# Optimization experiments

Hardware: AMD Instinct MI355X
Metric: run time of the kernel (lower is better)

## Reference

```python
import jax, jax.numpy as jnp
import numpy as np

D = 1024        # d_model
H = 4           # num_heads
DK = D          # key_dim   (expand_k = 1.0)
DV = 2 * D      # value_dim (expand_v = 2.0)
HK = DK // H    # per-head key dim
HV = DV // H    # per-head value dim
KCONV = 4       # short conv kernel size
EPS = 1e-5
CHUNK = 64      # scan chunk size (checkpointing granularity)


def causal_conv_silu(x, w):
    # x: [B,T,C], w: [C,K] depthwise causal conv followed by silu
    B, T, C = x.shape
    K = w.shape[1]
    xp = jnp.pad(x, ((0, 0), (K - 1, 0), (0, 0)))
    y = sum(xp[:, i:i + T, :] * w[:, i] for i in range(K))
    return jax.nn.silu(y)


def l2norm(x):
    return x * jax.lax.rsqrt(jnp.sum(x * x, -1, keepdims=True) + 1e-6)


def _step(S, inp):
    # gated delta rule, one time step. S: [B,H,HK,HV]
    q_t, k_t, v_t, g_t, b_t = inp  # [B,H,HK],[B,H,HK],[B,H,HV],[B,H],[B,H]
    S = S * jnp.exp(g_t)[..., None, None]
    v_eff = (v_t - jnp.einsum('bhk,bhkv->bhv', k_t, S)) * b_t[..., None]
    S = S + k_t[..., None] * v_eff[..., None, :]
    o_t = jnp.einsum('bhk,bhkv->bhv', q_t, S)
    return S, o_t


@jax.checkpoint
def _chunk(S, ch):
    return jax.lax.scan(_step, S, ch)


def _forward(x, ln_w, ln_b, Wq, Wk, Wv, conv_q, conv_k, conv_v, Wb, Wa,
             A_log, dt_bias, Wg, norm_w, Wo):
    B, T, _ = x.shape
    # pre-LayerNorm
    mu = jnp.mean(x, -1, keepdims=True)
    var = jnp.mean((x - mu) ** 2, -1, keepdims=True)
    normed = (x - mu) * jax.lax.rsqrt(var + EPS) * ln_w + ln_b
    # projections + short conv + silu
    q = causal_conv_silu(normed @ Wq, conv_q)
    k = causal_conv_silu(normed @ Wk, conv_k)
    v = causal_conv_silu(normed @ Wv, conv_v)
    beta = jax.nn.sigmoid(normed @ Wb)                                # [B,T,H]
    g = -jnp.exp(A_log) * jax.nn.softplus(normed @ Wa + dt_bias)      # [B,T,H]
    q = l2norm(q.reshape(B, T, H, HK)) * (HK ** -0.5)
    k = l2norm(k.reshape(B, T, H, HK))
    v = v.reshape(B, T, H, HV)
    # chunked sequential scan over time
    nc = T // CHUNK
    def to_chunks(a):
        return jnp.moveaxis(a, 1, 0).reshape((nc, CHUNK, B) + a.shape[2:])
    qc, kc, vc, gc, bc = map(to_chunks, (q, k, v, g, beta))
    S0 = jnp.zeros((B, H, HK, HV), x.dtype)
    _, o = jax.lax.scan(_chunk, S0, (qc, kc, vc, gc, bc))
    o = jnp.moveaxis(o.reshape(T, B, H, HV), 0, 1)                    # [B,T,H,HV]
    # RMSNorm-swish output gate
    g_out = (normed @ Wg).reshape(B, T, H, HV)
    o = o * jax.lax.rsqrt(jnp.mean(o * o, -1, keepdims=True) + EPS) * norm_w
    o = o * g_out * jax.nn.sigmoid(g_out)
    return x + o.reshape(B, T, DV) @ Wo


def setup_inputs() -> dict:
    key = jax.random.key(0)
    ks = jax.random.split(key, 16)
    B, T = 4, 2048
    p = lambda k, shape, s=0.02: jax.random.normal(k, shape, jnp.float32) * s
    return {
        'x': jax.random.normal(ks[0], (B, T, D), jnp.float32),
        'ln_w': jnp.ones((D,), jnp.float32),
        'ln_b': jnp.zeros((D,), jnp.float32),
        'Wq': p(ks[1], (D, DK)),
        'Wk': p(ks[2], (D, DK)),
        'Wv': p(ks[3], (D, DV)),
        'conv_q': p(ks[4], (DK, KCONV), 0.1),
        'conv_k': p(ks[5], (DK, KCONV), 0.1),
        'conv_v': p(ks[6], (DV, KCONV), 0.1),
        'Wb': p(ks[7], (D, H)),
        'Wa': p(ks[8], (D, H)),
        'A_log': jnp.log(jax.random.uniform(ks[9], (H,), jnp.float32, 1.0, 16.0)),
        'dt_bias': jnp.log(jnp.expm1(jax.random.uniform(ks[10], (H,), jnp.float32, 0.001, 0.1))),
        'Wg': p(ks[11], (D, DV)),
        'norm_w': jnp.ones((HV,), jnp.float32),
        'Wo': p(ks[12], (DV, D)),
    }


def reference(x, ln_w, ln_b, Wq, Wk, Wv, conv_q, conv_k, conv_v, Wb, Wa,
              A_log, dt_bias, Wg, norm_w, Wo):
    return _forward(x, ln_w, ln_b, Wq, Wk, Wv, conv_q, conv_k, conv_v,
                    Wb, Wa, A_log, dt_bias, Wg, norm_w, Wo)
```

## Files before the change

### kernel.cpp

```cpp
#include <hip/hip_runtime.h>
#include <math.h>

#define BB 4
#define TT 2048
#define RTOT 8192
#define DD 1024
#define HH 4
#define DKC 1024
#define DVC 2048
#define HKC 256
#define HVC 512
#define NC 32
#define TILE_CV 32

typedef unsigned short u16;
typedef unsigned int u32;
typedef short bf8v __attribute__((ext_vector_type(8)));
typedef float f32x4 __attribute__((ext_vector_type(4)));

__device__ __forceinline__ float bf2f(u16 u) {
    union { float f; u32 i; } c; c.i = ((u32)u) << 16; return c.f;
}
__device__ __forceinline__ u16 f2bf(float f) {
    union { float f; u32 i; } c; c.f = f;
    const u32 i = c.i;
    return (u16)((i + 0x7FFFu + ((i >> 16) & 1u)) >> 16);
}
__device__ __forceinline__ float sigmoidf_(float x) { return 1.0f / (1.0f + expf(-x)); }
__device__ __forceinline__ f32x4 mfma16(bf8v a, bf8v b, f32x4 c) {
    return __builtin_amdgcn_mfma_f32_16x16x32_bf16(a, b, c, 0, 0, 0);
}

__global__ __launch_bounds__(256) void ln_kernel(const float* __restrict__ x,
                                                 const float* __restrict__ w,
                                                 const float* __restrict__ b,
                                                 u16* __restrict__ out) {
    const int row = blockIdx.x;
    const int tid = threadIdx.x;
    const int lane = tid & 63, wave = tid >> 6;
    const float4 xv = *(const float4*)&x[(size_t)row * DD + tid * 4];
    float s = xv.x + xv.y + xv.z + xv.w;
    float sq = xv.x * xv.x + xv.y * xv.y + xv.z * xv.z + xv.w * xv.w;
    for (int m = 32; m >= 1; m >>= 1) {
        s += __shfl_xor(s, m, 64);
        sq += __shfl_xor(sq, m, 64);
    }
    __shared__ float s1[4], s2[4];
    if (lane == 0) { s1[wave] = s; s2[wave] = sq; }
    __syncthreads();
    const float tot = s1[0] + s1[1] + s1[2] + s1[3];
    const float totq = s2[0] + s2[1] + s2[2] + s2[3];
    const float mean = tot * (1.0f / DD);
    const float var = totq * (1.0f / DD) - mean * mean;
    const float rstd = rsqrtf(var + 1e-5f);
    const float4 wv = *(const float4*)&w[tid * 4];
    const float4 bv = *(const float4*)&b[tid * 4];
    ushort4 o;
    o.x = f2bf((xv.x - mean) * rstd * wv.x + bv.x);
    o.y = f2bf((xv.y - mean) * rstd * wv.y + bv.y);
    o.z = f2bf((xv.z - mean) * rstd * wv.z + bv.z);
    o.w = f2bf((xv.w - mean) * rstd * wv.w + bv.w);
    *(ushort4*)&out[(size_t)row * DD + tid * 4] = o;
}

__global__ __launch_bounds__(256) void wconv_kernel(const float* __restrict__ W,
                                                    u16* __restrict__ WT, int K, int N) {
    __shared__ float tile[32][33];
    const int k0 = blockIdx.x * 32, n0 = blockIdx.y * 32;
    const int t = threadIdx.x;
    const int r = t >> 3, c4 = (t & 7) * 4;
    const float4 v = *(const float4*)&W[(size_t)(k0 + r) * N + n0 + c4];
    tile[r][c4 + 0] = v.x; tile[r][c4 + 1] = v.y;
    tile[r][c4 + 2] = v.z; tile[r][c4 + 3] = v.w;
    __syncthreads();
    ushort4 o;
    o.x = f2bf(tile[c4 + 0][r]); o.y = f2bf(tile[c4 + 1][r]);
    o.z = f2bf(tile[c4 + 2][r]); o.w = f2bf(tile[c4 + 3][r]);
    *(ushort4*)&WT[(size_t)(n0 + r) * K + k0 + c4] = o;
}

template <int OUTMODE>
__global__ __launch_bounds__(256, 2) void gemm_mfma(const u16* __restrict__ A,
                                                    const u16* __restrict__ BT,
                                                    void* __restrict__ Cv,
                                                    int M, int N, int K,
                                                    const float* __restrict__ Res) {
    __shared__ u16 As[128][40];
    __shared__ u16 Bs[128][40];
    const int tid = threadIdx.x;
    const int wave = tid >> 6, lane = tid & 63;
    const int quad = lane >> 4, l15 = lane & 15;
    const int wr = wave >> 1, wc = wave & 1;
    const int bn = blockIdx.x, bm = blockIdx.y;
    const int srow = tid >> 1, sh = (tid & 1) * 16;
    const u16* Ap = A + (size_t)(bm * 128 + srow) * K + sh;
    const u16* Bp = BT + (size_t)(bn * 128 + srow) * K + sh;
    f32x4 acc[4][4];
#pragma unroll
    for (int i = 0; i < 4; ++i)
#pragma unroll
        for (int j = 0; j < 4; ++j) acc[i][j] = (f32x4){0.f, 0.f, 0.f, 0.f};

    for (int k0 = 0; k0 < K; k0 += 32) {
        const bf8v a0 = *(const bf8v*)(Ap + k0);
        const bf8v a1 = *(const bf8v*)(Ap + k0 + 8);
        const bf8v b0 = *(const bf8v*)(Bp + k0);
        const bf8v b1 = *(const bf8v*)(Bp + k0 + 8);
        __syncthreads();
        *(bf8v*)&As[srow][sh] = a0;
        *(bf8v*)&As[srow][sh + 8] = a1;
        *(bf8v*)&Bs[srow][sh] = b0;
        *(bf8v*)&Bs[srow][sh + 8] = b1;
        __syncthreads();
        bf8v af[4], bfr[4];
#pragma unroll
        for (int i = 0; i < 4; ++i) af[i] = *(const bf8v*)&As[wr * 64 + i * 16 + l15][quad * 8];
#pragma unroll
        for (int j = 0; j < 4; ++j) bfr[j] = *(const bf8v*)&Bs[wc * 64 + j * 16 + l15][quad * 8];
#pragma unroll
        for (int i = 0; i < 4; ++i)
#pragma unroll
            for (int j = 0; j < 4; ++j)
                acc[i][j] = mfma16(af[i], bfr[j], acc[i][j]);
    }
#pragma unroll
    for (int i = 0; i < 4; ++i) {
        const int row = bm * 128 + wr * 64 + i * 16 + quad * 4;
#pragma unroll
        for (int j = 0; j < 4; ++j) {
            const int col = bn * 128 + wc * 64 + j * 16 + l15;
            if (OUTMODE == 0) {
                u16* C = (u16*)Cv;
#pragma unroll
                for (int r = 0; r < 4; ++r)
                    C[(size_t)(row + r) * N + col] = f2bf(acc[i][j][r]);
            } else {
                float* C = (float*)Cv;
#pragma unroll
                for (int r = 0; r < 4; ++r)
                    C[(size_t)(row + r) * N + col] = acc[i][j][r] + Res[(size_t)(row + r) * N + col];
            }
        }
    }
}

__global__ __launch_bounds__(256) void smallproj_kernel(const float* __restrict__ x,
                                                        const float* __restrict__ lnw,
                                                        const float* __restrict__ lnb,
                                                        const float* __restrict__ Wb,
                                                        const float* __restrict__ Wa,
                                                        const float* __restrict__ A_log,
                                                        const float* __restrict__ dt_bias,
                                                        float* __restrict__ beta,
                                                        float* __restrict__ gdec) {
    const int row = blockIdx.x;
    const int tid = threadIdx.x;
    const int lane = tid & 63, wave = tid >> 6;
    const float4 xv = *(const float4*)&x[(size_t)row * DD + tid * 4];
    float s = xv.x + xv.y + xv.z + xv.w;
    float sq = xv.x * xv.x + xv.y * xv.y + xv.z * xv.z + xv.w * xv.w;
    for (int m = 32; m >= 1; m >>= 1) {
        s += __shfl_xor(s, m, 64);
        sq += __shfl_xor(sq, m, 64);
    }
    __shared__ float s1[4], s2[4];
    if (lane == 0) { s1[wave] = s; s2[wave] = sq; }
    __syncthreads();
    const float mean = (s1[0] + s1[1] + s1[2] + s1[3]) * (1.0f / DD);
    const float var = (s2[0] + s2[1] + s2[2] + s2[3]) * (1.0f / DD) - mean * mean;
    const float rstd = rsqrtf(var + 1e-5f);
    const float4 wv = *(const float4*)&lnw[tid * 4];
    const float4 bv = *(const float4*)&lnb[tid * 4];
    float nv[4];
    nv[0] = (xv.x - mean) * rstd * wv.x + bv.x;
    nv[1] = (xv.y - mean) * rstd * wv.y + bv.y;
    nv[2] = (xv.z - mean) * rstd * wv.z + bv.z;
    nv[3] = (xv.w - mean) * rstd * wv.w + bv.w;
    float acc[8] = {};
#pragma unroll
    for (int j = 0; j < 4; ++j) {
        const int kk = tid * 4 + j;
        const float4 wb = ((const float4*)Wb)[kk];
        const float4 wa = ((const float4*)Wa)[kk];
        acc[0] += nv[j] * wb.x; acc[1] += nv[j] * wb.y; acc[2] += nv[j] * wb.z; acc[3] += nv[j] * wb.w;
        acc[4] += nv[j] * wa.x; acc[5] += nv[j] * wa.y; acc[6] += nv[j] * wa.z; acc[7] += nv[j] * wa.w;
    }
#pragma unroll
    for (int i = 0; i < 8; ++i)
        for (int m = 32; m >= 1; m >>= 1) acc[i] += __shfl_xor(acc[i], m, 64);
    __shared__ float sred[4][8];
    if (lane == 0)
#pragma unroll
        for (int i = 0; i < 8; ++i) sred[wave][i] = acc[i];
    __syncthreads();
    if (tid < 8) {
        const float sv = sred[0][tid] + sred[1][tid] + sred[2][tid] + sred[3][tid];
        if (tid < 4) {
            beta[(size_t)row * HH + tid] = 1.0f / (1.0f + expf(-sv));
        } else {
            const int h = tid - 4;
            const float z = sv + dt_bias[h];
            const float sp = (z > 20.0f) ? z : log1pf(expf(z));
            gdec[(size_t)row * HH + h] = -expf(A_log[h]) * sp;
        }
    }
}

__global__ __launch_bounds__(256) void halo_save(const u16* __restrict__ P,
                                                 u16* __restrict__ halo, int C) {
    const int tt = blockIdx.x;
    const int r0 = tt * TILE_CV;
    const int t0 = r0 & (TT - 1);
    const int n4 = (3 * C) >> 2;
    for (int idx = threadIdx.x; idx < n4; idx += 256) {
        const int flat = idx * 4;
        const int j = flat / C;
        const int c = flat - j * C;
        ushort4 vv;
        if (t0 == 0) { vv.x = vv.y = vv.z = vv.w = 0; }
        else vv = *(const ushort4*)&P[(size_t)(r0 - 1 - j) * C + c];
        *(ushort4*)&halo[(size_t)(tt * 3 + j) * C + c] = vv;
    }
}

__global__ __launch_bounds__(256) void conv_inplace(u16* __restrict__ P,
                                                    const float* __restrict__ w,
                                                    const u16* __restrict__ halo, int C) {
    const int tt = blockIdx.y;
    const int r0 = tt * TILE_CV;
    const int c0 = blockIdx.x * 1024 + threadIdx.x * 4;
    float wt[4][4];
#pragma unroll
    for (int j = 0; j < 4; ++j)
#pragma unroll
        for (int i = 0; i < 4; ++i) wt[j][i] = w[(c0 + j) * 4 + i];
    float xm1[4], xm2[4], xm3[4];
    {
        const ushort4 h0 = *(const ushort4*)&halo[(size_t)(tt * 3 + 0) * C + c0];
        const ushort4 h1 = *(const ushort4*)&halo[(size_t)(tt * 3 + 1) * C + c0];
        const ushort4 h2 = *(const ushort4*)&halo[(size_t)(tt * 3 + 2) * C + c0];
        xm1[0] = bf2f(h0.x); xm1[1] = bf2f(h0.y); xm1[2] = bf2f(h0.z); xm1[3] = bf2f(h0.w);
        xm2[0] = bf2f(h1.x); xm2[1] = bf2f(h1.y); xm2[2] = bf2f(h1.z); xm2[3] = bf2f(h1.w);
        xm3[0] = bf2f(h2.x); xm3[1] = bf2f(h2.y); xm3[2] = bf2f(h2.z); xm3[3] = bf2f(h2.w);
    }
    for (int t = 0; t < TILE_CV; ++t) {
        u16* rowp = P + (size_t)(r0 + t) * C + c0;
        const ushort4 cv = *(const ushort4*)rowp;
        float cur[4] = {bf2f(cv.x), bf2f(cv.y), bf2f(cv.z), bf2f(cv.w)};
        ushort4 ov;
        u16* op = (u16*)&ov;
#pragma unroll
        for (int j = 0; j < 4; ++j) {
            const float y = xm3[j] * wt[j][0] + xm2[j] * wt[j][1] + xm1[j] * wt[j][2] + cur[j] * wt[j][3];
            op[j] = f2bf(y * sigmoidf_(y));
        }
        *(ushort4*)rowp = ov;
#pragma unroll
        for (int j = 0; j < 4; ++j) { xm3[j] = xm2[j]; xm2[j] = xm1[j]; xm1[j] = cur[j]; }
    }
}

__global__ __launch_bounds__(256) void normqk_kernel(u16* __restrict__ q, u16* __restrict__ k) {
    const int row = blockIdx.x;
    const int tid = threadIdx.x;
    const int h = tid >> 6, lane = tid & 63;
    const size_t base = (size_t)row * DKC + h * HKC + lane * 4;
    const ushort4 q4 = *(ushort4*)&q[base];
    const ushort4 k4 = *(ushort4*)&k[base];
    float qv[4] = {bf2f(q4.x), bf2f(q4.y), bf2f(q4.z), bf2f(q4.w)};
    float kv[4] = {bf2f(k4.x), bf2f(k4.y), bf2f(k4.z), bf2f(k4.w)};
    float sq = qv[0]*qv[0] + qv[1]*qv[1] + qv[2]*qv[2] + qv[3]*qv[3];
    float sk = kv[0]*kv[0] + kv[1]*kv[1] + kv[2]*kv[2] + kv[3]*kv[3];
    for (int m = 32; m >= 1; m >>= 1) {
        sq += __shfl_xor(sq, m, 64);
        sk += __shfl_xor(sk, m, 64);
    }
    const float qs = rsqrtf(sq + 1e-6f) * 0.0625f;
    const float ks = rsqrtf(sk + 1e-6f);
    ushort4 qo, ko;
    qo.x = f2bf(qv[0]*qs); qo.y = f2bf(qv[1]*qs); qo.z = f2bf(qv[2]*qs); qo.w = f2bf(qv[3]*qs);
    ko.x = f2bf(kv[0]*ks); ko.y = f2bf(kv[1]*ks); ko.z = f2bf(kv[2]*ks); ko.w = f2bf(kv[3]*ks);
    *(ushort4*)&q[base] = qo;
    *(ushort4*)&k[base] = ko;
}

__global__ __launch_bounds__(256) void p1a_kernel(const u16* __restrict__ qg,
                                                  const u16* __restrict__ kg,
                                                  const float* __restrict__ gdec,
                                                  const float* __restrict__ beta,
                                                  u16* __restrict__ Mg,
                                                  u16* __restrict__ Pg,
                                                  float* __restrict__ gcg) {
    __shared__ float T[64][68];
    __shared__ float Mm[64][68];
    __shared__ float gcs[64], bars[64];
    const int CI = blockIdx.x;
    const int c = CI & 31, h = (CI >> 5) & 3, b = CI >> 7;
    const int tid = threadIdx.x, lane = tid & 63, wave = tid >> 6;
    const int quad = lane >> 4, l15 = lane & 15;
    const int rowbase = b * TT + c * 64;
    if (wave == 0) {
        float g = gdec[(size_t)(rowbase + lane) * HH + h];
        for (int d = 1; d < 64; d <<= 1) { float o2 = __shfl_up(g, d, 64); if (lane >= d) g += o2; }
        gcs[lane] = g;
        bars[lane] = beta[(size_t)(rowbase + lane) * HH + h];
        gcg[CI * 64 + lane] = g;
    }
    __syncthreads();
    const int t0 = wave * 16;
    f32x4 kk[4], qk[4];
#pragma unroll
    for (int st = 0; st < 4; ++st) { kk[st] = (f32x4){0,0,0,0}; qk[st] = (f32x4){0,0,0,0}; }
    const size_t arow = (size_t)(rowbase + t0 + l15) * DKC + h * HKC + quad * 8;
    for (int ks = 0; ks < 8; ++ks) {
        const bf8v ak = *(const bf8v*)(kg + arow + ks * 32);
        const bf8v aq = *(const bf8v*)(qg + arow + ks * 32);
#pragma unroll
        for (int st = 0; st < 4; ++st) {
            const size_t brow = (size_t)(rowbase + st * 16 + l15) * DKC + h * HKC + quad * 8 + ks * 32;
            const bf8v bk = *(const bf8v*)(kg + brow);
            kk[st] = mfma16(ak, bk, kk[st]);
            qk[st] = mfma16(aq, bk, qk[st]);
        }
    }
#pragma unroll
    for (int st = 0; st < 4; ++st)
#pragma unroll
        for (int i = 0; i < 4; ++i) {
            const int t = t0 + quad * 4 + i, s = st * 16 + l15;
            const float e = expf(gcs[t] - gcs[s]);
            T[t][s] = (s < t) ? bars[t] * e * kk[st][i] : 0.f;
            Pg[(size_t)CI * 4096 + t * 64 + s] = f2bf((s <= t) ? e * qk[st][i] : 0.f);
        }
    __syncthreads();
    if (wave == 0) {
        const int j = lane;
        Mm[0][j] = (j == 0) ? 1.f : 0.f;
        for (int t = 1; t < 64; ++t) {
            float acc = 0.f;
            for (int s = 0; s < t; ++s) acc += T[t][s] * Mm[s][j];
            Mm[t][j] = ((t == j) ? 1.f : 0.f) - acc;
        }
    }
    __syncthreads();
    for (int idx = tid; idx < 4096; idx += 256)
        Mg[(size_t)CI * 4096 + idx] = f2bf(Mm[idx >> 6][idx & 63]);
}

__global__ __launch_bounds__(256) void p2_kernel(const u16* __restrict__ qg,
                                                 const u16* __restrict__ kg,
                                                 const u16* __restrict__ vg,
                                                 const float* __restrict__ beta,
                                                 const float* __restrict__ gcg,
                                                 const u16* __restrict__ Mg,
                                                 const u16* __restrict__ Pg,
                                                 u16* __restrict__ og) {
    __shared__ u16 SbT[32][264];
    __shared__ u16 buf[18432];
    __shared__ u16 tT[32][72];
    __shared__ float barr[64], negbg[64], gamt[64], gcdg[64];
    __shared__ float gCsh;
    const int bid = blockIdx.x;
    const int vs = bid & 15, h = (bid >> 4) & 3, b = bid >> 6;
    const int tid = threadIdx.x, lane = tid & 63, wave = tid >> 6;
    const int quad = lane >> 4, l15 = lane & 15;
    const int t0 = wave * 16;
    for (int i = tid; i < 32 * 264; i += 256) ((u16*)SbT)[i] = 0;
    f32x4 S[4][2];
#pragma unroll
    for (int a = 0; a < 4; ++a)
#pragma unroll
        for (int nb = 0; nb < 2; ++nb) S[a][nb] = (f32x4){0,0,0,0};

    const int srow = tid >> 2, scq = tid & 3;

    for (int c = 0; c < NC; ++c) {
        const int CI = (b * 4 + h) * NC + c;
        const int rowbase = b * TT + c * 64;
        __syncthreads();
        if (wave == 0) {
            const float gc = gcg[CI * 64 + lane];
            const float gc63 = __shfl(gc, 63, 64);
            const float bt = beta[(size_t)(rowbase + lane) * HH + h];
            const float gt = expf(gc);
            barr[lane] = bt; gamt[lane] = gt;
            negbg[lane] = -bt * gt;
            gcdg[lane] = expf(gc63 - gc);
            if (lane == 0) gCsh = expf(gc63);
        }
        __syncthreads();
        {
            const float sc = negbg[srow];
            const u16* krow = kg + (size_t)(rowbase + srow) * DKC + h * HKC + scq * 64;
            u16* dst = buf + srow * 264 + scq * 64;
#pragma unroll
            for (int it = 0; it < 8; ++it) {
                const ushort4 a0 = *(const ushort4*)(krow + it * 8);
                const ushort4 a1 = *(const ushort4*)(krow + it * 8 + 4);
                ushort4 o0, o1;
                o0.x = f2bf(bf2f(a0.x)*sc); o0.y = f2bf(bf2f(a0.y)*sc);
                o0.z = f2bf(bf2f(a0.z)*sc); o0.w = f2bf(bf2f(a0.w)*sc);
                o1.x = f2bf(bf2f(a1.x)*sc); o1.y = f2bf(bf2f(a1.y)*sc);
                o1.z = f2bf(bf2f(a1.z)*sc); o1.w = f2bf(bf2f(a1.w)*sc);
                *(ushort4*)(dst + it * 8) = o0;
                *(ushort4*)(dst + it * 8 + 4) = o1;
            }
        }
        __syncthreads();
        f32x4 uacc[2];
#pragma unroll
        for (int nb = 0; nb < 2; ++nb) {
            f32x4 ci;
#pragma unroll
            for (int i = 0; i < 4; ++i) {
                const int t = t0 + quad * 4 + i;
                ci[i] = barr[t] * bf2f(vg[(size_t)(rowbase + t) * DVC + h * HVC + vs * 32 + nb * 16 + l15]);
            }
            uacc[nb] = ci;
        }
        for (int ks = 0; ks < 8; ++ks) {
            const bf8v af = *(const bf8v*)(buf + (t0 + l15) * 264 + ks * 32 + quad * 8);
#pragma unroll
            for (int nb = 0; nb < 2; ++nb) {
                const bf8v bf_ = *(const bf8v*)(&SbT[nb * 16 + l15][ks * 32 + quad * 8]);
                uacc[nb] = mfma16(af, bf_, uacc[nb]);
            }
        }
#pragma unroll
        for (int nb = 0; nb < 2; ++nb) {
            ushort4 p;
            p.x = f2bf(uacc[nb][0]); p.y = f2bf(uacc[nb][1]);
            p.z = f2bf(uacc[nb][2]); p.w = f2bf(uacc[nb][3]);
            *(ushort4*)(&tT[nb * 16 + l15][t0 + quad * 4]) = p;
        }
        __syncthreads();
        f32x4 vacc[2] = {(f32x4){0,0,0,0}, (f32x4){0,0,0,0}};
        for (int ks = 0; ks < 2; ++ks) {
            const bf8v am = *(const bf8v*)(Mg + (size_t)CI * 4096 + (t0 + l15) * 64 + ks * 32 + quad * 8);
#pragma unroll
            for (int nb = 0; nb < 2; ++nb) {
                const bf8v bu = *(const bf8v*)(&tT[nb * 16 + l15][ks * 32 + quad * 8]);
                vacc[nb] = mfma16(am, bu, vacc[nb]);
            }
        }
        {
            const float sc = gamt[srow];
            const u16* qrow = qg + (size_t)(rowbase + srow) * DKC + h * HKC + scq * 64;
            u16* dst = buf + srow * 264 + scq * 64;
#pragma unroll
            for (int it = 0; it < 8; ++it) {
                const ushort4 a0 = *(const ushort4*)(qrow + it * 8);
                const ushort4 a1 = *(const ushort4*)(qrow + it * 8 + 4);
                ushort4 o0, o1;
                o0.x = f2bf(bf2f(a0.x)*sc); o0.y = f2bf(bf2f(a0.y)*sc);
                o0.z = f2bf(bf2f(a0.z)*sc); o0.w = f2bf(bf2f(a0.w)*sc);
                o1.x = f2bf(bf2f(a1.x)*sc); o1.y = f2bf(bf2f(a1.y)*sc);
                o1.z = f2bf(bf2f(a1.z)*sc); o1.w = f2bf(bf2f(a1.w)*sc);
                *(ushort4*)(dst + it * 8) = o0;
                *(ushort4*)(dst + it * 8 + 4) = o1;
            }
        }
        __syncthreads();
#pragma unroll
        for (int nb = 0; nb < 2; ++nb) {
            ushort4 p;
            p.x = f2bf(vacc[nb][0]); p.y = f2bf(vacc[nb][1]);
            p.z = f2bf(vacc[nb][2]); p.w = f2bf(vacc[nb][3]);
            *(ushort4*)(&tT[nb * 16 + l15][t0 + quad * 4]) = p;
        }
        __syncthreads();
        f32x4 oacc[2] = {(f32x4){0,0,0,0}, (f32x4){0,0,0,0}};
        for (int ks = 0; ks < 2; ++ks) {
            const bf8v ap = *(const bf8v*)(Pg + (size_t)CI * 4096 + (t0 + l15) * 64 + ks * 32 + quad * 8);
#pragma unroll
            for (int nb = 0; nb < 2; ++nb) {
                const bf8v bv_ = *(const bf8v*)(&tT[nb * 16 + l15][ks * 32 + quad * 8]);
                oacc[nb] = mfma16(ap, bv_, oacc[nb]);
            }
        }
        for (int ks = 0; ks < 8; ++ks) {
            const bf8v af = *(const bf8v*)(buf + (t0 + l15) * 264 + ks * 32 + quad * 8);
#pragma unroll
            for (int nb = 0; nb < 2; ++nb) {
                const bf8v bs = *(const bf8v*)(&SbT[nb * 16 + l15][ks * 32 + quad * 8]);
                oacc[nb] = mfma16(af, bs, oacc[nb]);
            }
        }
#pragma unroll
        for (int nb = 0; nb < 2; ++nb)
#pragma unroll
            for (int i = 0; i < 4; ++i) {
                const int t = t0 + quad * 4 + i;
                og[((size_t)(b * 4 + h) * TT + c * 64 + t) * HVC + vs * 32 + nb * 16 + l15] = f2bf(oacc[nb][i]);
            }
        __syncthreads();
        {
            const float sc = gcdg[srow];
            const u16* krow = kg + (size_t)(rowbase + srow) * DKC + h * HKC + scq * 64;
#pragma unroll
            for (int it = 0; it < 8; ++it) {
                const ushort4 a0 = *(const ushort4*)(krow + it * 8);
                const ushort4 a1 = *(const ushort4*)(krow + it * 8 + 4);
                const int cbase = scq * 64 + it * 8;
                buf[(cbase + 0) * 72 + srow] = f2bf(bf2f(a0.x)*sc);
                buf[(cbase + 1) * 72 + srow] = f2bf(bf2f(a0.y)*sc);
                buf[(cbase + 2) * 72 + srow] = f2bf(bf2f(a0.z)*sc);
                buf[(cbase + 3) * 72 + srow] = f2bf(bf2f(a0.w)*sc);
                buf[(cbase + 4) * 72 + srow] = f2bf(bf2f(a1.x)*sc);
                buf[(cbase + 5) * 72 + srow] = f2bf(bf2f(a1.y)*sc);
                buf[(cbase + 6) * 72 + srow] = f2bf(bf2f(a1.z)*sc);
                buf[(cbase + 7) * 72 + srow] = f2bf(bf2f(a1.w)*sc);
            }
        }
        __syncthreads();
        const float gC = gCsh;
#pragma unroll
        for (int a = 0; a < 4; ++a) {
            const int r0 = (wave * 4 + a) * 16;
#pragma unroll
            for (int nb = 0; nb < 2; ++nb) {
                f32x4 acc = S[a][nb] * gC;
                for (int ks = 0; ks < 2; ++ks) {
                    const bf8v akt = *(const bf8v*)(buf + (r0 + l15) * 72 + ks * 32 + quad * 8);
                    const bf8v bv_ = *(const bf8v*)(&tT[nb * 16 + l15][ks * 32 + quad * 8]);
                    acc = mfma16(akt, bv_, acc);
                }
                S[a][nb] = acc;
                ushort4 p;
                p.x = f2bf(acc[0]); p.y = f2bf(acc[1]);
                p.z = f2bf(acc[2]); p.w = f2bf(acc[3]);
                *(ushort4*)(&SbT[nb * 16 + l15][r0 + quad * 4]) = p;
            }
        }
    }
}

__global__ __launch_bounds__(256) void gate_kernel(const u16* __restrict__ o,
                                                   u16* __restrict__ pg,
                                                   const float* __restrict__ norm_w) {
    const int row = blockIdx.x;
    const int b = row >> 11, t = row & 2047;
    const int tid = threadIdx.x;
    const int h = tid >> 6, lane = tid & 63;
    const size_t obase = ((size_t)(b * 4 + h) * TT + t) * HVC + lane * 4;
    const size_t pbase = (size_t)row * DVC + h * HVC + lane * 4;
    const ushort4 a4 = *(const ushort4*)&o[obase];
    const ushort4 b4 = *(const ushort4*)&o[obase + 256];
    float o1[4] = {bf2f(a4.x), bf2f(a4.y), bf2f(a4.z), bf2f(a4.w)};
    float o2[4] = {bf2f(b4.x), bf2f(b4.y), bf2f(b4.z), bf2f(b4.w)};
    float ss = 0.f;
#pragma unroll
    for (int j = 0; j < 4; ++j) ss += o1[j]*o1[j] + o2[j]*o2[j];
    for (int m = 32; m >= 1; m >>= 1) ss += __shfl_xor(ss, m, 64);
    const float rms = rsqrtf(ss * (1.0f / HVC) + 1e-5f);
    const float4 nw1 = *(const float4*)&norm_w[lane * 4];
    const float4 nw2 = *(const float4*)&norm_w[256 + lane * 4];
    const ushort4 g4a = *(const ushort4*)&pg[pbase];
    const ushort4 g4b = *(const ushort4*)&pg[pbase + 256];
    const float g1[4] = {bf2f(g4a.x), bf2f(g4a.y), bf2f(g4a.z), bf2f(g4a.w)};
    const float g2[4] = {bf2f(g4b.x), bf2f(g4b.y), bf2f(g4b.z), bf2f(g4b.w)};
    const float n1[4] = {nw1.x, nw1.y, nw1.z, nw1.w};
    const float n2[4] = {nw2.x, nw2.y, nw2.z, nw2.w};
    ushort4 r1, r2;
    u16* p1 = (u16*)&r1; u16* p2 = (u16*)&r2;
#pragma unroll
    for (int j = 0; j < 4; ++j) {
        p1[j] = f2bf(o1[j] * rms * n1[j] * g1[j] * sigmoidf_(g1[j]));
        p2[j] = f2bf(o2[j] * rms * n2[j] * g2[j] * sigmoidf_(g2[j]));
    }
    *(ushort4*)&pg[pbase] = r1;
    *(ushort4*)&pg[pbase + 256] = r2;
}

extern "C" void kernel_launch(void* const* d_in, const int* in_sizes, int n_in,
                              void* d_out, int out_size, void* d_ws, size_t ws_size,
                              hipStream_t stream) {
    const float* x       = (const float*)d_in[0];
    const float* ln_w    = (const float*)d_in[1];
    const float* ln_b    = (const float*)d_in[2];
    const float* Wq      = (const float*)d_in[3];
    const float* Wk      = (const float*)d_in[4];
    const float* Wv      = (const float*)d_in[5];
    const float* conv_q  = (const float*)d_in[6];
    const float* conv_k  = (const float*)d_in[7];
    const float* conv_v  = (const float*)d_in[8];
    const float* Wb      = (const float*)d_in[9];
    const float* Wa      = (const float*)d_in[10];
    const float* A_log   = (const float*)d_in[11];
    const float* dt_bias = (const float*)d_in[12];
    const float* Wg      = (const float*)d_in[13];
    const float* norm_w  = (const float*)d_in[14];
    const float* Wo      = (const float*)d_in[15];
    float* out = (float*)d_out;

    char* ws = (char*)d_ws;
    u16* normed = (u16*)(ws);
    u16* q      = (u16*)(ws + (16ull << 20));
    u16* k      = (u16*)(ws + (32ull << 20));
    u16* v      = (u16*)(ws + (48ull << 20));
    u16* o      = (u16*)(ws + (80ull << 20));
    float* beta = (float*)(ws + (112ull << 20));
    float* gdec = (float*)(ws + (112ull << 20) + (128u<<10));
    float* gcg  = (float*)(ws + (112ull << 20) + (256u<<10));
    u16* halo   = (u16*)(ws + (113ull << 20));
    u16* Mg     = (u16*)(ws + (116ull << 20));
    u16* Pg     = (u16*)(ws + (120ull << 20));
    u16* pg     = q;
    u16* WTe    = o;
    u16* WgT    = Mg;
    u16* WoT    = v;

    ln_kernel<<<RTOT, 256, 0, stream>>>(x, ln_w, ln_b, normed);

    wconv_kernel<<<dim3(DD / 32, DKC / 32), 256, 0, stream>>>(Wq, WTe, DD, DKC);
    gemm_mfma<0><<<dim3(DKC / 128, RTOT / 128), 256, 0, stream>>>(normed, WTe, q, RTOT, DKC, DD, nullptr);
    wconv_kernel<<<dim3(DD / 32, DKC / 32), 256, 0, stream>>>(Wk, WTe, DD, DKC);
    gemm_mfma<0><<<dim3(DKC / 128, RTOT / 128), 256, 0, stream>>>(normed, WTe, k, RTOT, DKC, DD, nullptr);
    wconv_kernel<<<dim3(DD / 32, DVC / 32), 256, 0, stream>>>(Wv, WTe, DD, DVC);
    gemm_mfma<0><<<dim3(DVC / 128, RTOT / 128), 256, 0, stream>>>(normed, WTe, v, RTOT, DVC, DD, nullptr);
    smallproj_kernel<<<RTOT, 256, 0, stream>>>(x, ln_w, ln_b, Wb, Wa, A_log, dt_bias, beta, gdec);

    halo_save<<<RTOT / TILE_CV, 256, 0, stream>>>(q, halo, DKC);
    conv_inplace<<<dim3(1, RTOT / TILE_CV), 256, 0, stream>>>(q, conv_q, halo, DKC);
    halo_save<<<RTOT / TILE_CV, 256, 0, stream>>>(k, halo, DKC);
    conv_inplace<<<dim3(1, RTOT / TILE_CV), 256, 0, stream>>>(k, conv_k, halo, DKC);
    halo_save<<<RTOT / TILE_CV, 256, 0, stream>>>(v, halo, DVC);
    conv_inplace<<<dim3(2, RTOT / TILE_CV), 256, 0, stream>>>(v, conv_v, halo, DVC);

    normqk_kernel<<<RTOT, 256, 0, stream>>>(q, k);

    p1a_kernel<<<BB * HH * NC, 256, 0, stream>>>(q, k, gdec, beta, Mg, Pg, gcg);
    p2_kernel<<<BB * HH * (HVC / 32), 256, 0, stream>>>(q, k, v, beta, gcg, Mg, Pg, o);

    wconv_kernel<<<dim3(DD / 32, DVC / 32), 256, 0, stream>>>(Wg, WgT, DD, DVC);
    gemm_mfma<0><<<dim3(DVC / 128, RTOT / 128), 256, 0, stream>>>(normed, WgT, pg, RTOT, DVC, DD, nullptr);

    gate_kernel<<<RTOT, 256, 0, stream>>>(o, pg, norm_w);

    wconv_kernel<<<dim3(DVC / 32, DD / 32), 256, 0, stream>>>(Wo, WoT, DVC, DD);
    gemm_mfma<1><<<dim3(DD / 128, RTOT / 128), 256, 0, stream>>>(pg, WoT, out, RTOT, DD, DVC, x);
}
```

Before: 792.5 us.

## Restructure chunk recurrence kernel with double-buffered state and precomputed transposed keys

```diff
diff --git a/kernel.cpp b/kernel.cpp
--- a/kernel.cpp
+++ b/kernel.cpp
@@ -290,6 +290,7 @@
                                                   const float* __restrict__ beta,
                                                   u16* __restrict__ Mg,
                                                   u16* __restrict__ Pg,
+                                                  u16* __restrict__ kTg,
                                                   float* __restrict__ gcg) {
     __shared__ float T[64][68];
     __shared__ float Mm[64][68];
@@ -308,6 +309,12 @@
     }
     __syncthreads();
     const int t0 = wave * 16;
+    bf8v I0, I16;
+#pragma unroll
+    for (int j = 0; j < 8; ++j) {
+        ((u16*)&I0)[j]  = (quad * 8 + j == l15)      ? (u16)0x3F80 : (u16)0;
+        ((u16*)&I16)[j] = (quad * 8 + j == l15 + 16) ? (u16)0x3F80 : (u16)0;
+    }
     f32x4 kk[4], qk[4];
 #pragma unroll
     for (int st = 0; st < 4; ++st) { kk[st] = (f32x4){0,0,0,0}; qk[st] = (f32x4){0,0,0,0}; }
@@ -315,6 +322,15 @@
     for (int ks = 0; ks < 8; ++ks) {
         const bf8v ak = *(const bf8v*)(kg + arow + ks * 32);
         const bf8v aq = *(const bf8v*)(qg + arow + ks * 32);
+        f32x4 tr0 = (f32x4){0,0,0,0}, tr1 = (f32x4){0,0,0,0};
+        tr0 = mfma16(I0, ak, tr0);
+        tr1 = mfma16(I16, ak, tr1);
+        const size_t kbase = (size_t)CI * 16384 + t0 + l15;
+#pragma unroll
+        for (int i = 0; i < 4; ++i) {
+            kTg[kbase + (size_t)(ks * 32 + quad * 4 + i) * 64] = f2bf(tr0[i]);
+            kTg[kbase + (size_t)(ks * 32 + 16 + quad * 4 + i) * 64] = f2bf(tr1[i]);
+        }
 #pragma unroll
         for (int st = 0; st < 4; ++st) {
             const size_t brow = (size_t)(rowbase + st * 16 + l15) * DKC + h * HKC + quad * 8 + ks * 32;
@@ -347,191 +363,123 @@
         Mg[(size_t)CI * 4096 + idx] = f2bf(Mm[idx >> 6][idx & 63]);
 }
 
-__global__ __launch_bounds__(256) void p2_kernel(const u16* __restrict__ qg,
+__global__ __launch_bounds__(512) void p2_kernel(const u16* __restrict__ qg,
                                                  const u16* __restrict__ kg,
                                                  const u16* __restrict__ vg,
                                                  const float* __restrict__ beta,
                                                  const float* __restrict__ gcg,
                                                  const u16* __restrict__ Mg,
                                                  const u16* __restrict__ Pg,
+                                                 const u16* __restrict__ kTg,
                                                  u16* __restrict__ og) {
-    __shared__ u16 SbT[32][264];
-    __shared__ u16 buf[18432];
-    __shared__ u16 tT[32][72];
-    __shared__ float barr[64], negbg[64], gamt[64], gcdg[64];
-    __shared__ float gCsh;
+    __shared__ u16 SbT[2][32][264];
+    __shared__ u16 uT[32][72];
+    __shared__ u16 vT[32][72];
+    __shared__ u16 v2T[32][72];
     const int bid = blockIdx.x;
     const int vs = bid & 15, h = (bid >> 4) & 3, b = bid >> 6;
     const int tid = threadIdx.x, lane = tid & 63, wave = tid >> 6;
     const int quad = lane >> 4, l15 = lane & 15;
-    const int t0 = wave * 16;
-    for (int i = tid; i < 32 * 264; i += 256) ((u16*)SbT)[i] = 0;
-    f32x4 S[4][2];
-#pragma unroll
-    for (int a = 0; a < 4; ++a)
-#pragma unroll
-        for (int nb = 0; nb < 2; ++nb) S[a][nb] = (f32x4){0,0,0,0};
-
-    const int srow = tid >> 2, scq = tid & 3;
+    const int tw = wave >> 1, nw = wave & 1;
+    const int t0 = tw * 16;
+    const int ncol = nw * 16 + l15;
+    for (int i = tid; i < 32 * 264; i += 512) ((u16*)SbT[0])[i] = 0;
+    f32x4 S[4];
+#pragma unroll
+    for (int a = 0; a < 4; ++a) S[a] = (f32x4){0,0,0,0};
+    __syncthreads();
 
     for (int c = 0; c < NC; ++c) {
+        const int cur = c & 1, nxt = cur ^ 1;
         const int CI = (b * 4 + h) * NC + c;
         const int rowbase = b * TT + c * 64;
-        __syncthreads();
-        if (wave == 0) {
-            const float gc = gcg[CI * 64 + lane];
-            const float gc63 = __shfl(gc, 63, 64);
-            const float bt = beta[(size_t)(rowbase + lane) * HH + h];
-            const float gt = expf(gc);
-            barr[lane] = bt; gamt[lane] = gt;
-            negbg[lane] = -bt * gt;
-            gcdg[lane] = expf(gc63 - gc);
-            if (lane == 0) gCsh = expf(gc63);
-        }
-        __syncthreads();
+        const float gc63 = gcg[CI * 64 + 63];
+        float bt[4], ga[4], gd[4];
+#pragma unroll
+        for (int i = 0; i < 4; ++i) {
+            const int t = t0 + quad * 4 + i;
+            bt[i] = beta[(size_t)(rowbase + t) * HH + h];
+            const float gc = gcg[CI * 64 + t];
+            ga[i] = expf(gc);
+            gd[i] = expf(gc63 - gc);
+        }
+        const size_t krow = (size_t)(rowbase + t0 + l15) * DKC + h * HKC + quad * 8;
+        f32x4 ka0 = (f32x4){0,0,0,0}, ka1 = (f32x4){0,0,0,0};
+        for (int ks = 0; ks < 8; ks += 2) {
+            const bf8v ak0 = *(const bf8v*)(kg + krow + ks * 32);
+            const bf8v ak1 = *(const bf8v*)(kg + krow + ks * 32 + 32);
+            const bf8v bs0 = *(const bf8v*)(&SbT[cur][ncol][ks * 32 + quad * 8]);
+            const bf8v bs1 = *(const bf8v*)(&SbT[cur][ncol][ks * 32 + 32 + quad * 8]);
+            ka0 = mfma16(ak0, bs0, ka0);
+            ka1 = mfma16(ak1, bs1, ka1);
+        }
         {
-            const float sc = negbg[srow];
-            const u16* krow = kg + (size_t)(rowbase + srow) * DKC + h * HKC + scq * 64;
-            u16* dst = buf + srow * 264 + scq * 64;
-#pragma unroll
-            for (int it = 0; it < 8; ++it) {
-                const ushort4 a0 = *(const ushort4*)(krow + it * 8);
-                const ushort4 a1 = *(const ushort4*)(krow + it * 8 + 4);
-                ushort4 o0, o1;
-                o0.x = f2bf(bf2f(a0.x)*sc); o0.y = f2bf(bf2f(a0.y)*sc);
-                o0.z = f2bf(bf2f(a0.z)*sc); o0.w = f2bf(bf2f(a0.w)*sc);
-                o1.x = f2bf(bf2f(a1.x)*sc); o1.y = f2bf(bf2f(a1.y)*sc);
-                o1.z = f2bf(bf2f(a1.z)*sc); o1.w = f2bf(bf2f(a1.w)*sc);
-                *(ushort4*)(dst + it * 8) = o0;
-                *(ushort4*)(dst + it * 8 + 4) = o1;
-            }
-        }
-        __syncthreads();
-        f32x4 uacc[2];
-#pragma unroll
-        for (int nb = 0; nb < 2; ++nb) {
-            f32x4 ci;
+            ushort4 up; u16* upp = (u16*)&up;
 #pragma unroll
             for (int i = 0; i < 4; ++i) {
                 const int t = t0 + quad * 4 + i;
-                ci[i] = barr[t] * bf2f(vg[(size_t)(rowbase + t) * DVC + h * HVC + vs * 32 + nb * 16 + l15]);
+                const float vv = bf2f(vg[(size_t)(rowbase + t) * DVC + h * HVC + vs * 32 + ncol]);
+                upp[i] = f2bf(bt[i] * vv - bt[i] * ga[i] * (ka0[i] + ka1[i]));
             }
-            uacc[nb] = ci;
-        }
-        for (int ks = 0; ks < 8; ++ks) {
-            const bf8v af = *(const bf8v*)(buf + (t0 + l15) * 264 + ks * 32 + quad * 8);
-#pragma unroll
-            for (int nb = 0; nb < 2; ++nb) {
-                const bf8v bf_ = *(const bf8v*)(&SbT[nb * 16 + l15][ks * 32 + quad * 8]);
-                uacc[nb] = mfma16(af, bf_, uacc[nb]);
-            }
-        }
-#pragma unroll
-        for (int nb = 0; nb < 2; ++nb) {
-            ushort4 p;
-            p.x = f2bf(uacc[nb][0]); p.y = f2bf(uacc[nb][1]);
-            p.z = f2bf(uacc[nb][2]); p.w = f2bf(uacc[nb][3]);
-            *(ushort4*)(&tT[nb * 16 + l15][t0 + quad * 4]) = p;
+            *(ushort4*)(&uT[ncol][t0 + quad * 4]) = up;
         }
         __syncthreads();
-        f32x4 vacc[2] = {(f32x4){0,0,0,0}, (f32x4){0,0,0,0}};
+        f32x4 vacc = (f32x4){0,0,0,0};
         for (int ks = 0; ks < 2; ++ks) {
             const bf8v am = *(const bf8v*)(Mg + (size_t)CI * 4096 + (t0 + l15) * 64 + ks * 32 + quad * 8);
-#pragma unroll
-            for (int nb = 0; nb < 2; ++nb) {
-                const bf8v bu = *(const bf8v*)(&tT[nb * 16 + l15][ks * 32 + quad * 8]);
-                vacc[nb] = mfma16(am, bu, vacc[nb]);
+            const bf8v bu = *(const bf8v*)(&uT[ncol][ks * 32 + quad * 8]);
+            vacc = mfma16(am, bu, vacc);
+        }
+        {
+            ushort4 vp, v2p; u16* vpp = (u16*)&vp; u16* v2pp = (u16*)&v2p;
+#pragma unroll
+            for (int i = 0; i < 4; ++i) {
+                vpp[i] = f2bf(vacc[i]);
+                v2pp[i] = f2bf(vacc[i] * gd[i]);
             }
-        }
-        {
-            const float sc = gamt[srow];
-            const u16* qrow = qg + (size_t)(rowbase + srow) * DKC + h * HKC + scq * 64;
-            u16* dst = buf + srow * 264 + scq * 64;
-#pragma unroll
-            for (int it = 0; it < 8; ++it) {
-                const ushort4 a0 = *(const ushort4*)(qrow + it * 8);
-                const ushort4 a1 = *(const ushort4*)(qrow + it * 8 + 4);
-                ushort4 o0, o1;
-                o0.x = f2bf(bf2f(a0.x)*sc); o0.y = f2bf(bf2f(a0.y)*sc);
-                o0.z = f2bf(bf2f(a0.z)*sc); o0.w = f2bf(bf2f(a0.w)*sc);
-                o1.x = f2bf(bf2f(a1.x)*sc); o1.y = f2bf(bf2f(a1.y)*sc);
-                o1.z = f2bf(bf2f(a1.z)*sc); o1.w = f2bf(bf2f(a1.w)*sc);
-                *(ushort4*)(dst + it * 8) = o0;
-                *(ushort4*)(dst + it * 8 + 4) = o1;
-            }
+            *(ushort4*)(&vT[ncol][t0 + quad * 4]) = vp;
+            *(ushort4*)(&v2T[ncol][t0 + quad * 4]) = v2p;
         }
         __syncthreads();
-#pragma unroll
-        for (int nb = 0; nb < 2; ++nb) {
-            ushort4 p;
-            p.x = f2bf(vacc[nb][0]); p.y = f2bf(vacc[nb][1]);
-            p.z = f2bf(vacc[nb][2]); p.w = f2bf(vacc[nb][3]);
-            *(ushort4*)(&tT[nb * 16 + l15][t0 + quad * 4]) = p;
-        }
-        __syncthreads();
-        f32x4 oacc[2] = {(f32x4){0,0,0,0}, (f32x4){0,0,0,0}};
+        f32x4 op_ = (f32x4){0,0,0,0};
         for (int ks = 0; ks < 2; ++ks) {
             const bf8v ap = *(const bf8v*)(Pg + (size_t)CI * 4096 + (t0 + l15) * 64 + ks * 32 + quad * 8);
-#pragma unroll
-            for (int nb = 0; nb < 2; ++nb) {
-                const bf8v bv_ = *(const bf8v*)(&tT[nb * 16 + l15][ks * 32 + quad * 8]);
-                oacc[nb] = mfma16(ap, bv_, oacc[nb]);
+            const bf8v bv_ = *(const bf8v*)(&vT[ncol][ks * 32 + quad * 8]);
+            op_ = mfma16(ap, bv_, op_);
+        }
+        f32x4 oq0 = (f32x4){0,0,0,0}, oq1 = (f32x4){0,0,0,0};
+        const size_t qrow = (size_t)(rowbase + t0 + l15) * DKC + h * HKC + quad * 8;
+        for (int ks = 0; ks < 8; ks += 2) {
+            const bf8v aq0 = *(const bf8v*)(qg + qrow + ks * 32);
+            const bf8v aq1 = *(const bf8v*)(qg + qrow + ks * 32 + 32);
+            const bf8v bs0 = *(const bf8v*)(&SbT[cur][ncol][ks * 32 + quad * 8]);
+            const bf8v bs1 = *(const bf8v*)(&SbT[cur][ncol][ks * 32 + 32 + quad * 8]);
+            oq0 = mfma16(aq0, bs0, oq0);
+            oq1 = mfma16(aq1, bs1, oq1);
+        }
+#pragma unroll
+        for (int i = 0; i < 4; ++i) {
+            const int t = t0 + quad * 4 + i;
+            og[((size_t)(b * 4 + h) * TT + c * 64 + t) * HVC + vs * 32 + ncol] =
+                f2bf(op_[i] + ga[i] * (oq0[i] + oq1[i]));
+        }
+        const float gC = expf(gc63);
+#pragma unroll
+        for (int a = 0; a < 4; ++a) {
+            const int r0 = (tw * 4 + a) * 16;
+            f32x4 acc = S[a] * gC;
+            for (int ks = 0; ks < 2; ++ks) {
+                const bf8v akt = *(const bf8v*)(kTg + (size_t)CI * 16384 + (r0 + l15) * 64 + ks * 32 + quad * 8);
+                const bf8v bv2 = *(const bf8v*)(&v2T[ncol][ks * 32 + quad * 8]);
+                acc = mfma16(akt, bv2, acc);
             }
-        }
-        for (int ks = 0; ks < 8; ++ks) {
-            const bf8v af = *(const bf8v*)(buf + (t0 + l15) * 264 + ks * 32 + quad * 8);
-#pragma unroll
-            for (int nb = 0; nb < 2; ++nb) {
-                const bf8v bs = *(const bf8v*)(&SbT[nb * 16 + l15][ks * 32 + quad * 8]);
-                oacc[nb] = mfma16(af, bs, oacc[nb]);
-            }
-        }
-#pragma unroll
-        for (int nb = 0; nb < 2; ++nb)
-#pragma unroll
-            for (int i = 0; i < 4; ++i) {
-                const int t = t0 + quad * 4 + i;
-                og[((size_t)(b * 4 + h) * TT + c * 64 + t) * HVC + vs * 32 + nb * 16 + l15] = f2bf(oacc[nb][i]);
-            }
+            S[a] = acc;
+            ushort4 sp; u16* spp = (u16*)&sp;
+#pragma unroll
+            for (int i = 0; i < 4; ++i) spp[i] = f2bf(acc[i]);
+            *(ushort4*)(&SbT[nxt][ncol][r0 + quad * 4]) = sp;
+        }
         __syncthreads();
-        {
-            const float sc = gcdg[srow];
-            const u16* krow = kg + (size_t)(rowbase + srow) * DKC + h * HKC + scq * 64;
-#pragma unroll
-            for (int it = 0; it < 8; ++it) {
-                const ushort4 a0 = *(const ushort4*)(krow + it * 8);
-                const ushort4 a1 = *(const ushort4*)(krow + it * 8 + 4);
-                const int cbase = scq * 64 + it * 8;
-                buf[(cbase + 0) * 72 + srow] = f2bf(bf2f(a0.x)*sc);
-                buf[(cbase + 1) * 72 + srow] = f2bf(bf2f(a0.y)*sc);
-                buf[(cbase + 2) * 72 + srow] = f2bf(bf2f(a0.z)*sc);
-                buf[(cbase + 3) * 72 + srow] = f2bf(bf2f(a0.w)*sc);
-                buf[(cbase + 4) * 72 + srow] = f2bf(bf2f(a1.x)*sc);
-                buf[(cbase + 5) * 72 + srow] = f2bf(bf2f(a1.y)*sc);
-                buf[(cbase + 6) * 72 + srow] = f2bf(bf2f(a1.z)*sc);
-                buf[(cbase + 7) * 72 + srow] = f2bf(bf2f(a1.w)*sc);
-            }
-        }
-        __syncthreads();
-        const float gC = gCsh;
-#pragma unroll
-        for (int a = 0; a < 4; ++a) {
-            const int r0 = (wave * 4 + a) * 16;
-#pragma unroll
-            for (int nb = 0; nb < 2; ++nb) {
-                f32x4 acc = S[a][nb] * gC;
-                for (int ks = 0; ks < 2; ++ks) {
-                    const bf8v akt = *(const bf8v*)(buf + (r0 + l15) * 72 + ks * 32 + quad * 8);
-                    const bf8v bv_ = *(const bf8v*)(&tT[nb * 16 + l15][ks * 32 + quad * 8]);
-                    acc = mfma16(akt, bv_, acc);
-                }
-                S[a][nb] = acc;
-                ushort4 p;
-                p.x = f2bf(acc[0]); p.y = f2bf(acc[1]);
-                p.z = f2bf(acc[2]); p.w = f2bf(acc[3]);
-                *(ushort4*)(&SbT[nb * 16 + l15][r0 + quad * 4]) = p;
-            }
-        }
     }
 }
 
@@ -609,6 +557,7 @@
     u16* WTe    = o;
     u16* WgT    = Mg;
     u16* WoT    = v;
+    u16* kTg    = (u16*)d_out;
 
     ln_kernel<<<RTOT, 256, 0, stream>>>(x, ln_w, ln_b, normed);
 
@@ -629,8 +578,8 @@
 
     normqk_kernel<<<RTOT, 256, 0, stream>>>(q, k);
 
-    p1a_kernel<<<BB * HH * NC, 256, 0, stream>>>(q, k, gdec, beta, Mg, Pg, gcg);
-    p2_kernel<<<BB * HH * (HVC / 32), 256, 0, stream>>>(q, k, v, beta, gcg, Mg, Pg, o);
+    p1a_kernel<<<BB * HH * NC, 256, 0, stream>>>(q, k, gdec, beta, Mg, Pg, kTg, gcg);
+    p2_kernel<<<BB * HH * (HVC / 32), 512, 0, stream>>>(q, k, v, beta, gcg, Mg, Pg, kTg, o);
 
     wconv_kernel<<<dim3(DD / 32, DVC / 32), 256, 0, stream>>>(Wg, WgT, DD, DVC);
     gemm_mfma<0><<<dim3(DVC / 128, RTOT / 128), 256, 0, stream>>>(normed, WgT, pg, RTOT, DVC, DD, nullptr);
```

Measured after the change: 793.1 us. About the same (+0.1%).
